# Kernel optimization log

Measured on AMD Instinct MI355X. Metric: run time of the kernel, lower is better.

The kernel has to match this reference:

```python
import jax, jax.numpy as jnp
import numpy as np

N_TRACKS = 2048          # chunk_size = 32*32*2 in the source
CONF_THRESHOLD = 3.0     # conf_threshold default
NORM_INLIER_THRESH = 0.01  # reprojection inlier threshold in normalized camera coords
PIX_THRESH = 1.5         # frame-0 pixel reprojection threshold from the source
MIN_TRI_INLIER = 4       # min_tri_inlier_num default


def setup_inputs() -> dict:
    key = jax.random.key(0)
    k1, k2, k3 = jax.random.split(key, 3)
    S, H, W = 8, 224, 224
    pts = jax.random.normal(k1, (S, H, W, 3), dtype=jnp.float32)
    # confidences in (1, 5) so (conf - 3 + 0.5) weights span negative/positive as in the source
    conf = 1.0 + 4.0 * jax.random.uniform(k2, (S, H, W), dtype=jnp.float32)
    K = jnp.array([[300.0, 0.0, W / 2.0], [0.0, 300.0, H / 2.0], [0.0, 0.0, 1.0]], dtype=jnp.float32)
    intrinsics = jnp.tile(K[None], (S, 1, 1))
    w2cs = jnp.tile(jnp.eye(4, dtype=jnp.float32)[None], (S, 1, 1))
    w2cs = w2cs.at[:, :3, 3].set(0.1 * jax.random.normal(k3, (S, 3), dtype=jnp.float32))
    return {"pts": pts, "conf": conf, "intrinsics": intrinsics, "w2cs": w2cs}


def reference(pts, conf, intrinsics, w2cs):
    S, H, W, _ = pts.shape
    HW = H * W
    pts_flat = pts.reshape(S, HW, 3)
    conf_flat = conf.reshape(S, HW)

    # --- sample N reference points in frame 0 by confidence (fixed-size analogue of quantile mask) ---
    _, idx0 = jax.lax.top_k(conf_flat[0], N_TRACKS)          # [N]
    ref = pts_flat[0, idx0]                                   # [N,3]
    ref_sq = (ref ** 2).sum(-1)                               # [N]

    # --- brute-force pairwise sq-dist + argmin match, per frame (memory-bound core) ---
    def match(frame_pts):  # frame_pts: [HW,3]
        d = ref_sq[:, None] - 2.0 * (ref @ frame_pts.T) + (frame_pts ** 2).sum(-1)[None, :]  # [N,HW]
        return jnp.argmin(d, axis=1)

    matches_rest = jax.lax.map(match, pts_flat[1:])           # [S-1,N]
    matches = jnp.concatenate([idx0[None], matches_rest], 0)  # [S,N]

    xs = (matches % W).astype(pts.dtype)
    ys = (matches // W).astype(pts.dtype)
    track_xy = jnp.stack([xs, ys], -1)                        # [S,N,2] (x,y) per source reorder [...,[1,0]]
    track_conf = jnp.take_along_axis(conf_flat, matches, axis=1)  # [S,N]

    # --- normalize tracks by intrinsics ---
    pp = intrinsics[:, :2, 2][:, None, :]                     # [S,1,2]
    f = jnp.stack([intrinsics[:, 0, 0], intrinsics[:, 1, 1]], -1)[:, None, :]  # [S,1,2]
    tn = (track_xy - pp) / f                                  # [S,N,2]

    # --- weighted multi-view DLT triangulation (conf-weighted, per-point 4x4 eigh) ---
    wgt = track_conf - CONF_THRESHOLD + 0.5                   # [S,N]
    P = w2cs[:, :3, :]                                        # [S,3,4]
    r1 = (tn[..., 0:1] * P[:, None, 2, :] - P[:, None, 0, :]) * wgt[..., None]  # [S,N,4]
    r2 = (tn[..., 1:2] * P[:, None, 2, :] - P[:, None, 1, :]) * wgt[..., None]
    AtA = jnp.einsum('sni,snj->nij', r1, r1) + jnp.einsum('sni,snj->nij', r2, r2)  # [N,4,4]
    _, evecs = jnp.linalg.eigh(AtA)
    v = evecs[..., 0]                                         # eigvec of smallest eigval, [N,4]
    denom = jnp.where(jnp.abs(v[:, 3:4]) < 1e-8, 1e-8, v[:, 3:4])
    X = v[:, :3] / denom                                      # [N,3] triangulated points

    # --- per-view reprojection, inlier count ---
    Xc = jnp.einsum('sij,nj->sni', P[:, :, :3], X) + P[:, None, :, 3]  # [S,N,3]
    z = Xc[..., 2:3]
    z = jnp.where(jnp.abs(z) < 1e-6, 1e-6, z)
    uv = Xc[..., :2] / z                                      # [S,N,2] normalized
    err = jnp.linalg.norm(uv - tn, axis=-1)                   # [S,N]
    inlier = err < NORM_INLIER_THRESH                         # [S,N]
    inlier_num = inlier.sum(0)                                # [N] int32

    # --- frame-0 pixel reprojection mask (source: (pos - track_matches[0]).norm < 1.5 & inlier_num > S//2) ---
    pos = uv[0] * f[0] + pp[0]                                # [N,2] pixels
    err_px0 = jnp.linalg.norm(pos - track_xy[0], axis=-1)
    final_mask = (err_px0 < PIX_THRESH) & (inlier_num > S // 2)

    # --- points_conf as in batched_triangulate ---
    pconf = (track_conf * inlier).sum(0) / jnp.clip(inlier_num, 1)
    pconf = jnp.where(inlier_num >= MIN_TRI_INLIER, pconf, 1.0)

    return X, pconf, final_mask.astype(jnp.int32), inlier_num
```

## Files before the change

kernel.cpp:

```cpp
#include <hip/hip_runtime.h>
#include <math.h>

#define HW       50176
#define W_IMG    224
#define S_FRAMES 8
#define NT       2048
#define NJCH     98
#define JCH      512
#define TPC      2

__device__ unsigned           g_hist1[65536];
__device__ unsigned           g_hist2[65536];
__device__ unsigned           g_scalars[16];
__device__ unsigned long long g_keys[4096];
__device__ int                g_matches[S_FRAMES * NT];
__device__ float4             g_ref[NT];
__device__ float              g_pd[7 * NT * NJCH];
__device__ int                g_pj[7 * NT * NJCH];

__device__ __forceinline__ unsigned ordered_u32(float f) {
  unsigned u = __float_as_uint(f);
  return (u & 0x80000000u) ? ~u : (u | 0x80000000u);
}

__global__ void zero_kernel() {
  int i = blockIdx.x * blockDim.x + threadIdx.x;
  if (i < 65536) { g_hist1[i] = 0u; g_hist2[i] = 0u; }
  if (i < 4096)  g_keys[i] = 0ULL;
  if (i < 16)    g_scalars[i] = 0u;
}

__global__ void hist1_kernel(const float* __restrict__ conf) {
  int i = blockIdx.x * blockDim.x + threadIdx.x;
  if (i < HW) atomicAdd(&g_hist1[ordered_u32(conf[i]) >> 16], 1u);
}

__global__ __launch_bounds__(1024) void scan1_kernel() {
  __shared__ unsigned ssum[1024];
  int t = threadIdx.x;
  unsigned mysum = 0;
  for (int b = 0; b < 64; ++b) mysum += g_hist1[t * 64 + b];
  ssum[t] = mysum;
  __syncthreads();
  for (int off = 1; off < 1024; off <<= 1) {
    unsigned v = (t + off < 1024) ? ssum[t + off] : 0u;
    __syncthreads();
    ssum[t] += v;
    __syncthreads();
  }
  unsigned run = ssum[t] - mysum;
  for (int b = 63; b >= 0; --b) {
    unsigned h = g_hist1[t * 64 + b];
    if (run < NT && run + h >= NT) { g_scalars[0] = (unsigned)(t * 64 + b); g_scalars[1] = run; }
    run += h;
  }
}

__global__ void hist2_kernel(const float* __restrict__ conf) {
  int i = blockIdx.x * blockDim.x + threadIdx.x;
  if (i < HW) {
    unsigned ou = ordered_u32(conf[i]);
    if ((ou >> 16) == g_scalars[0]) atomicAdd(&g_hist2[ou & 0xFFFFu], 1u);
  }
}

__global__ __launch_bounds__(1024) void scan2_kernel() {
  __shared__ unsigned ssum[1024];
  int t = threadIdx.x;
  unsigned R = NT - g_scalars[1];
  unsigned mysum = 0;
  for (int b = 0; b < 64; ++b) mysum += g_hist2[t * 64 + b];
  ssum[t] = mysum;
  __syncthreads();
  for (int off = 1; off < 1024; off <<= 1) {
    unsigned v = (t + off < 1024) ? ssum[t + off] : 0u;
    __syncthreads();
    ssum[t] += v;
    __syncthreads();
  }
  unsigned run = ssum[t] - mysum;
  for (int b = 63; b >= 0; --b) {
    unsigned h = g_hist2[t * 64 + b];
    if (run < R && run + h >= R) g_scalars[2] = (g_scalars[0] << 16) | (unsigned)(t * 64 + b);
    run += h;
  }
}

__global__ void compact_kernel(const float* __restrict__ conf) {
  int i = blockIdx.x * blockDim.x + threadIdx.x;
  if (i < HW) {
    unsigned ou = ordered_u32(conf[i]);
    if (ou >= g_scalars[2]) {
      unsigned pos = atomicAdd(&g_scalars[4], 1u);
      if (pos < 4096) g_keys[pos] = ((unsigned long long)ou << 32) | (unsigned long long)(0xFFFFFFFFu - (unsigned)i);
    }
  }
}

__global__ __launch_bounds__(1024) void sortwrite_kernel(const float* __restrict__ pts) {
  __shared__ unsigned long long sk[4096];
  int t = threadIdx.x;
  for (int i = t; i < 4096; i += 1024) sk[i] = ~g_keys[i];
  for (unsigned k = 2; k <= 4096; k <<= 1) {
    for (unsigned j = k >> 1; j > 0; j >>= 1) {
      __syncthreads();
      for (unsigned i = t; i < 4096; i += 1024) {
        unsigned ixj = i ^ j;
        if (ixj > i) {
          unsigned long long a = sk[i], b = sk[ixj];
          bool up = ((i & k) == 0);
          if (up ? (a > b) : (a < b)) { sk[i] = b; sk[ixj] = a; }
        }
      }
    }
  }
  __syncthreads();
  for (int i = t; i < NT; i += 1024) {
    unsigned long long key = ~sk[i];
    unsigned idx = 0xFFFFFFFFu - (unsigned)(key & 0xFFFFFFFFu);
    g_matches[i] = (int)idx;
    const float* p = pts + (size_t)idx * 3;
    float x = p[0], y = p[1], z = p[2];
    g_ref[i] = make_float4(x, y, z, fmaf(x, x, fmaf(y, y, z * z)));
  }
}

__global__ __launch_bounds__(256) void match_kernel(const float* __restrict__ pts) {
  __shared__ float4 tile[256];
  int jc = blockIdx.x;
  int ic = blockIdx.y;
  int f  = blockIdx.z;
  int t  = threadIdx.x;
  int ib = ic * 1024 + t;

  float4 r0 = g_ref[ib];
  float4 r1 = g_ref[ib + 256];
  float4 r2 = g_ref[ib + 512];
  float4 r3 = g_ref[ib + 768];
  float dmin0 = INFINITY, dmin1 = INFINITY, dmin2 = INFINITY, dmin3 = INFINITY;
  int   jmin0 = 0, jmin1 = 0, jmin2 = 0, jmin3 = 0;

  const float* fp = pts + (size_t)(f + 1) * HW * 3;
  int jbase0 = jc * JCH;
  for (int ti = 0; ti < TPC; ++ti) {
    int jb = jbase0 + ti * 256;
    const float* p = fp + (size_t)(jb + t) * 3;
    float x = p[0], y = p[1], z = p[2];
    float sq = fmaf(x, x, fmaf(y, y, z * z));
    __syncthreads();
    tile[t] = make_float4(-2.0f * x, -2.0f * y, -2.0f * z, sq);
    __syncthreads();
#pragma unroll 4
    for (int u = 0; u < 256; ++u) {
      float4 q = tile[u];
      int ju = jb + u;
      float d0 = fmaf(q.x, r0.x, fmaf(q.y, r0.y, fmaf(q.z, r0.z, q.w)));
      float d1 = fmaf(q.x, r1.x, fmaf(q.y, r1.y, fmaf(q.z, r1.z, q.w)));
      float d2 = fmaf(q.x, r2.x, fmaf(q.y, r2.y, fmaf(q.z, r2.z, q.w)));
      float d3 = fmaf(q.x, r3.x, fmaf(q.y, r3.y, fmaf(q.z, r3.z, q.w)));
      if (d0 < dmin0) { dmin0 = d0; jmin0 = ju; }
      if (d1 < dmin1) { dmin1 = d1; jmin1 = ju; }
      if (d2 < dmin2) { dmin2 = d2; jmin2 = ju; }
      if (d3 < dmin3) { dmin3 = d3; jmin3 = ju; }
    }
  }
  int id0 = f * NT + ib;
  g_pd[(id0)       * NJCH + jc] = dmin0;  g_pj[(id0)       * NJCH + jc] = jmin0;
  g_pd[(id0 + 256) * NJCH + jc] = dmin1;  g_pj[(id0 + 256) * NJCH + jc] = jmin1;
  g_pd[(id0 + 512) * NJCH + jc] = dmin2;  g_pj[(id0 + 512) * NJCH + jc] = jmin2;
  g_pd[(id0 + 768) * NJCH + jc] = dmin3;  g_pj[(id0 + 768) * NJCH + jc] = jmin3;
}

__global__ void reduce_kernel() {
  int id = blockIdx.x * blockDim.x + threadIdx.x;
  if (id >= 7 * NT) return;
  float dmin = INFINITY;
  int   jmin = 0;
  for (int c = 0; c < NJCH; ++c) {
    float d = g_pd[id * NJCH + c];
    int   j = g_pj[id * NJCH + c];
    if (d < dmin) { dmin = d; jmin = j; }
  }
  int f = id / NT, i = id % NT;
  g_matches[(f + 1) * NT + i] = jmin;
}

__global__ void solve_kernel(const float* __restrict__ conf, const float* __restrict__ intr,
                             const float* __restrict__ w2cs, float* __restrict__ out) {
  int i = blockIdx.x * blockDim.x + threadIdx.x;
  if (i >= NT) return;

  float A1[10] = {0}, A2[10] = {0};
  float tnx[8], tny[8], cf[8];
  float x0 = 0.f, y0 = 0.f;

  for (int s = 0; s < S_FRAMES; ++s) {
    int m = g_matches[s * NT + i];
    float xs = (float)(m % W_IMG);
    float ys = (float)(m / W_IMG);
    float c  = conf[s * HW + m];
    float fx = intr[s * 9 + 0], fy = intr[s * 9 + 4];
    float cx = intr[s * 9 + 2], cy = intr[s * 9 + 5];
    float tx = (xs - cx) / fx;
    float ty = (ys - cy) / fy;
    float w  = (c - 3.0f) + 0.5f;
    const float* P = w2cs + s * 16;
    float r1[4], r2[4];
#pragma unroll
    for (int k = 0; k < 4; ++k) {
      r1[k] = (tx * P[8 + k] - P[k])     * w;
      r2[k] = (ty * P[8 + k] - P[4 + k]) * w;
    }
    int idx = 0;
#pragma unroll
    for (int a = 0; a < 4; ++a)
#pragma unroll
      for (int b = a; b < 4; ++b) {
        A1[idx] += r1[a] * r1[b];
        A2[idx] += r2[a] * r2[b];
        ++idx;
      }
    tnx[s] = tx; tny[s] = ty; cf[s] = c;
    if (s == 0) { x0 = xs; y0 = ys; }
  }

  double a[4][4], V[4][4];
  {
    int idx = 0;
#pragma unroll
    for (int p = 0; p < 4; ++p)
#pragma unroll
      for (int q = p; q < 4; ++q) {
        double v = (double)(A1[idx] + A2[idx]);
        a[p][q] = v; a[q][p] = v; ++idx;
      }
#pragma unroll
    for (int p = 0; p < 4; ++p)
#pragma unroll
      for (int q = 0; q < 4; ++q) V[p][q] = (p == q) ? 1.0 : 0.0;
  }

  for (int sweep = 0; sweep < 8; ++sweep) {
#pragma unroll
    for (int p = 0; p < 3; ++p)
#pragma unroll
      for (int q = p + 1; q < 4; ++q) {
        double apq = a[p][q];
        if (fabs(apq) <= 1e-40) continue;
        double theta = (a[q][q] - a[p][p]) / (2.0 * apq);
        double tt  = copysign(1.0, theta) / (fabs(theta) + sqrt(theta * theta + 1.0));
        double cth = 1.0 / sqrt(tt * tt + 1.0);
        double sth = tt * cth;
#pragma unroll
        for (int k = 0; k < 4; ++k) {
          double akp = a[p][k], akq = a[q][k];
          a[p][k] = cth * akp - sth * akq;
          a[q][k] = sth * akp + cth * akq;
        }
#pragma unroll
        for (int k = 0; k < 4; ++k) {
          double akp = a[k][p], akq = a[k][q];
          a[k][p] = cth * akp - sth * akq;
          a[k][q] = sth * akp + cth * akq;
        }
#pragma unroll
        for (int k = 0; k < 4; ++k) {
          double vkp = V[k][p], vkq = V[k][q];
          V[k][p] = cth * vkp - sth * vkq;
          V[k][q] = sth * vkp + cth * vkq;
        }
      }
  }

  int kmin = 0; double emin = a[0][0];
#pragma unroll
  for (int k = 1; k < 4; ++k) if (a[k][k] < emin) { emin = a[k][k]; kmin = k; }

  double vsel[4];
#pragma unroll
  for (int r = 0; r < 4; ++r) {
    double x = V[r][0];
    if (kmin == 1) x = V[r][1];
    if (kmin == 2) x = V[r][2];
    if (kmin == 3) x = V[r][3];
    vsel[r] = x;
  }
  float v0 = (float)vsel[0], v1 = (float)vsel[1], v2 = (float)vsel[2], v3 = (float)vsel[3];
  float denom = (fabsf(v3) < 1e-8f) ? 1e-8f : v3;
  float X0 = v0 / denom, X1 = v1 / denom, X2 = v2 / denom;

  int innum = 0; float wsum = 0.f; float u0x = 0.f, u0y = 0.f;
  for (int s = 0; s < S_FRAMES; ++s) {
    const float* P = w2cs + s * 16;
    float Xc0 = fmaf(P[2],  X2, fmaf(P[1], X1, P[0] * X0)) + P[3];
    float Xc1 = fmaf(P[6],  X2, fmaf(P[5], X1, P[4] * X0)) + P[7];
    float z   = fmaf(P[10], X2, fmaf(P[9], X1, P[8] * X0)) + P[11];
    if (fabsf(z) < 1e-6f) z = 1e-6f;
    float ux = Xc0 / z, uy = Xc1 / z;
    float dx = ux - tnx[s], dy = uy - tny[s];
    float e = sqrtf(dx * dx + dy * dy);
    bool in = e < 0.01f;
    if (in) { innum++; wsum += cf[s]; }
    if (s == 0) { u0x = ux; u0y = uy; }
  }
  float fx0 = intr[0], fy0 = intr[4], cx0 = intr[2], cy0 = intr[5];
  float posx = fmaf(u0x, fx0, cx0), posy = fmaf(u0y, fy0, cy0);
  float dxp = posx - x0, dyp = posy - y0;
  float epx = sqrtf(dxp * dxp + dyp * dyp);
  int mask = (epx < 1.5f && innum > 4) ? 1 : 0;
  float pconf = wsum / (float)((innum > 1) ? innum : 1);
  if (innum < 4) pconf = 1.0f;

  out[3 * i + 0] = X0;
  out[3 * i + 1] = X1;
  out[3 * i + 2] = X2;
  out[6144 + i]  = pconf;
  out[8192 + i]  = (float)mask;
  out[10240 + i] = (float)innum;
}

extern "C" void kernel_launch(void* const* d_in, const int* in_sizes, int n_in,
                              void* d_out, int out_size, void* d_ws, size_t ws_size,
                              hipStream_t stream) {
  const float* pts  = (const float*)d_in[0];
  const float* conf = (const float*)d_in[1];
  const float* intr = (const float*)d_in[2];
  const float* w2cs = (const float*)d_in[3];
  float* out = (float*)d_out;

  zero_kernel   <<<256, 256, 0, stream>>>();
  hist1_kernel  <<<196, 256, 0, stream>>>(conf);
  scan1_kernel  <<<1,  1024, 0, stream>>>();
  hist2_kernel  <<<196, 256, 0, stream>>>(conf);
  scan2_kernel  <<<1,  1024, 0, stream>>>();
  compact_kernel<<<196, 256, 0, stream>>>(conf);
  sortwrite_kernel<<<1, 1024, 0, stream>>>(pts);
  match_kernel  <<<dim3(NJCH, 2, 7), 256, 0, stream>>>(pts);
  reduce_kernel <<<56,  256, 0, stream>>>();
  solve_kernel  <<<8,  256, 0, stream>>>(conf, intr, w2cs, out);
}
```

Measured before the change: 400.3 us.

## Halve match chunk size, transpose partial layout, and reshape solve launch

Halves the per-block j-chunk in the match kernel, which doubles the grid and removes the inner tile loop and one barrier. Partial minima are stored chunk-major so the reduce kernel's loads coalesce across threads. The solve kernel now launches with 64-thread blocks across more blocks, disables unrolling of several loops, and cuts the Jacobi sweeps from 8 to 6. Fewer sweeps may leave the eigenvector less converged, and the reduce kernel now walks twice as many partials.

```diff
diff --git a/kernel.cpp b/kernel.cpp
--- a/kernel.cpp
+++ b/kernel.cpp
@@ -5,9 +5,9 @@
 #define W_IMG    224
 #define S_FRAMES 8
 #define NT       2048
-#define NJCH     98
-#define JCH      512
-#define TPC      2
+#define NJCH     196
+#define JCH      256
+#define NID      (7 * NT)
 
 __device__ unsigned           g_hist1[65536];
 __device__ unsigned           g_hist2[65536];
@@ -15,8 +15,8 @@
 __device__ unsigned long long g_keys[4096];
 __device__ int                g_matches[S_FRAMES * NT];
 __device__ float4             g_ref[NT];
-__device__ float              g_pd[7 * NT * NJCH];
-__device__ int                g_pj[7 * NT * NJCH];
+__device__ float              g_pd[NJCH * NID];
+__device__ int                g_pj[NJCH * NID];
 
 __device__ __forceinline__ unsigned ordered_u32(float f) {
   unsigned u = __float_as_uint(f);
@@ -141,51 +141,47 @@
   int   jmin0 = 0, jmin1 = 0, jmin2 = 0, jmin3 = 0;
 
   const float* fp = pts + (size_t)(f + 1) * HW * 3;
-  int jbase0 = jc * JCH;
-  for (int ti = 0; ti < TPC; ++ti) {
-    int jb = jbase0 + ti * 256;
-    const float* p = fp + (size_t)(jb + t) * 3;
-    float x = p[0], y = p[1], z = p[2];
-    float sq = fmaf(x, x, fmaf(y, y, z * z));
-    __syncthreads();
-    tile[t] = make_float4(-2.0f * x, -2.0f * y, -2.0f * z, sq);
-    __syncthreads();
+  int jb = jc * JCH;
+  const float* p = fp + (size_t)(jb + t) * 3;
+  float x = p[0], y = p[1], z = p[2];
+  float sq = fmaf(x, x, fmaf(y, y, z * z));
+  tile[t] = make_float4(-2.0f * x, -2.0f * y, -2.0f * z, sq);
+  __syncthreads();
 #pragma unroll 4
-    for (int u = 0; u < 256; ++u) {
-      float4 q = tile[u];
-      int ju = jb + u;
-      float d0 = fmaf(q.x, r0.x, fmaf(q.y, r0.y, fmaf(q.z, r0.z, q.w)));
-      float d1 = fmaf(q.x, r1.x, fmaf(q.y, r1.y, fmaf(q.z, r1.z, q.w)));
-      float d2 = fmaf(q.x, r2.x, fmaf(q.y, r2.y, fmaf(q.z, r2.z, q.w)));
-      float d3 = fmaf(q.x, r3.x, fmaf(q.y, r3.y, fmaf(q.z, r3.z, q.w)));
-      if (d0 < dmin0) { dmin0 = d0; jmin0 = ju; }
-      if (d1 < dmin1) { dmin1 = d1; jmin1 = ju; }
-      if (d2 < dmin2) { dmin2 = d2; jmin2 = ju; }
-      if (d3 < dmin3) { dmin3 = d3; jmin3 = ju; }
-    }
-  }
-  int id0 = f * NT + ib;
-  g_pd[(id0)       * NJCH + jc] = dmin0;  g_pj[(id0)       * NJCH + jc] = jmin0;
-  g_pd[(id0 + 256) * NJCH + jc] = dmin1;  g_pj[(id0 + 256) * NJCH + jc] = jmin1;
-  g_pd[(id0 + 512) * NJCH + jc] = dmin2;  g_pj[(id0 + 512) * NJCH + jc] = jmin2;
-  g_pd[(id0 + 768) * NJCH + jc] = dmin3;  g_pj[(id0 + 768) * NJCH + jc] = jmin3;
+  for (int u = 0; u < 256; ++u) {
+    float4 q = tile[u];
+    int ju = jb + u;
+    float d0 = fmaf(q.x, r0.x, fmaf(q.y, r0.y, fmaf(q.z, r0.z, q.w)));
+    float d1 = fmaf(q.x, r1.x, fmaf(q.y, r1.y, fmaf(q.z, r1.z, q.w)));
+    float d2 = fmaf(q.x, r2.x, fmaf(q.y, r2.y, fmaf(q.z, r2.z, q.w)));
+    float d3 = fmaf(q.x, r3.x, fmaf(q.y, r3.y, fmaf(q.z, r3.z, q.w)));
+    if (d0 < dmin0) { dmin0 = d0; jmin0 = ju; }
+    if (d1 < dmin1) { dmin1 = d1; jmin1 = ju; }
+    if (d2 < dmin2) { dmin2 = d2; jmin2 = ju; }
+    if (d3 < dmin3) { dmin3 = d3; jmin3 = ju; }
+  }
+  int idb = f * NT + ib;
+  g_pd[jc * NID + idb]       = dmin0;  g_pj[jc * NID + idb]       = jmin0;
+  g_pd[jc * NID + idb + 256] = dmin1;  g_pj[jc * NID + idb + 256] = jmin1;
+  g_pd[jc * NID + idb + 512] = dmin2;  g_pj[jc * NID + idb + 512] = jmin2;
+  g_pd[jc * NID + idb + 768] = dmin3;  g_pj[jc * NID + idb + 768] = jmin3;
 }
 
 __global__ void reduce_kernel() {
   int id = blockIdx.x * blockDim.x + threadIdx.x;
-  if (id >= 7 * NT) return;
+  if (id >= NID) return;
   float dmin = INFINITY;
   int   jmin = 0;
   for (int c = 0; c < NJCH; ++c) {
-    float d = g_pd[id * NJCH + c];
-    int   j = g_pj[id * NJCH + c];
+    float d = g_pd[c * NID + id];
+    int   j = g_pj[c * NID + id];
     if (d < dmin) { dmin = d; jmin = j; }
   }
   int f = id / NT, i = id % NT;
   g_matches[(f + 1) * NT + i] = jmin;
 }
 
-__global__ void solve_kernel(const float* __restrict__ conf, const float* __restrict__ intr,
+__global__ __launch_bounds__(64) void solve_kernel(const float* __restrict__ conf, const float* __restrict__ intr,
                              const float* __restrict__ w2cs, float* __restrict__ out) {
   int i = blockIdx.x * blockDim.x + threadIdx.x;
   if (i >= NT) return;
@@ -194,6 +190,7 @@
   float tnx[8], tny[8], cf[8];
   float x0 = 0.f, y0 = 0.f;
 
+#pragma unroll 1
   for (int s = 0; s < S_FRAMES; ++s) {
     int m = g_matches[s * NT + i];
     float xs = (float)(m % W_IMG);
@@ -240,7 +237,8 @@
       for (int q = 0; q < 4; ++q) V[p][q] = (p == q) ? 1.0 : 0.0;
   }
 
-  for (int sweep = 0; sweep < 8; ++sweep) {
+#pragma unroll 1
+  for (int sweep = 0; sweep < 6; ++sweep) {
 #pragma unroll
     for (int p = 0; p < 3; ++p)
 #pragma unroll
@@ -290,6 +288,7 @@
   float X0 = v0 / denom, X1 = v1 / denom, X2 = v2 / denom;
 
   int innum = 0; float wsum = 0.f; float u0x = 0.f, u0y = 0.f;
+#pragma unroll 1
   for (int s = 0; s < S_FRAMES; ++s) {
     const float* P = w2cs + s * 16;
     float Xc0 = fmaf(P[2],  X2, fmaf(P[1], X1, P[0] * X0)) + P[3];
@@ -337,5 +336,5 @@
   sortwrite_kernel<<<1, 1024, 0, stream>>>(pts);
   match_kernel  <<<dim3(NJCH, 2, 7), 256, 0, stream>>>(pts);
   reduce_kernel <<<56,  256, 0, stream>>>();
-  solve_kernel  <<<8,  256, 0, stream>>>(conf, intr, w2cs, out);
-}
+  solve_kernel  <<<32,  64, 0, stream>>>(conf, intr, w2cs, out);
+}
```

Measured after the change: 412.9 us. +3.2%, slower.
